# Kernel tuning notes

Measured on AMD Instinct MI355X. Metric: run time of the kernel, lower is better.

The kernel has to match this reference:

```python
import jax, jax.numpy as jnp
import numpy as np


def setup_inputs() -> dict:
    key = jax.random.key(0)
    k1, k2 = jax.random.split(key)
    N, M, C = 8192, 16384, 128
    features = jax.random.normal(k1, (N, 1, 1, C), dtype=jnp.float32)
    patch_memory = jax.random.normal(k2, (1, M, 1, C), dtype=jnp.float32)
    return {"features": features, "patch_memory": patch_memory}


def reference(features, patch_memory):
    # Faithful to: torch.norm(features - patch_memory, dim=3); torch.min(dim=1)
    # features: [N, 1, 1, C], patch_memory: [1, M, 1, C] -> broadcast diff [N, M, 1, C]
    # Avoid materializing the [N, M, C] diff tensor: use the GEMM expansion
    # ||a-b||^2 = ||a||^2 + ||b||^2 - 2 a.b (same math, efficient form).
    f = features.reshape(features.shape[0], features.shape[-1])       # [N, C]
    m = patch_memory.reshape(patch_memory.shape[1], patch_memory.shape[-1])  # [M, C]
    f2 = jnp.sum(f * f, axis=-1)   # [N]
    m2 = jnp.sum(m * m, axis=-1)   # [M]
    cross = jnp.einsum('nc,mc->nm', f, m)  # [N, M]
    d2 = f2[:, None] + m2[None, :] - 2.0 * cross
    distances = jnp.sqrt(jnp.maximum(d2, 0.0))       # [N, M] == norm over dim 3
    min_distances = jnp.min(distances, axis=1)       # min over memory dim (dim=1)
    # original keeps the trailing singleton patch dim -> [N, 1]
    return min_distances[:, None]
```

## Files before the change

kernel.cpp:

```cpp
#include <hip/hip_runtime.h>
#include <hip/hip_bf16.h>
#include <stdint.h>

#define N_ROWS 8192
#define M_ROWS 16384
#define CDIM 128
#define NTILE 16
#define BTROWS 128

typedef unsigned short u16;
typedef __attribute__((ext_vector_type(2))) unsigned short u16x2;
typedef __attribute__((ext_vector_type(8))) short bf16x8;
typedef __attribute__((ext_vector_type(4))) float f32x4;

static __device__ __forceinline__ u16 f2bf(float x) {
  union { float f; uint32_t u; } v; v.f = x;
  uint32_t u = v.u;
  uint32_t r = u + 0x7FFFu + ((u >> 16) & 1u);
  return (u16)(r >> 16);
}
static __device__ __forceinline__ float bf2f(u16 b) {
  union { uint32_t u; float f; } v; v.u = ((uint32_t)b) << 16;
  return v.f;
}

#define GLOAD_LDS(gsrc, ldst)                                                  \
  __builtin_amdgcn_global_load_lds(                                            \
      (const __attribute__((address_space(1))) uint32_t*)(gsrc),               \
      (__attribute__((address_space(3))) uint32_t*)(ldst), 16, 0, 0)

__global__ __launch_bounds__(256) void prep_kernel(
    const float* __restrict__ f, const float* __restrict__ m,
    u16* __restrict__ fb, u16* __restrict__ mb,
    float* __restrict__ f2, float* __restrict__ mh, int* __restrict__ mind2)
{
  const int row = blockIdx.x * 4 + (threadIdx.x >> 6);
  const int lane = threadIdx.x & 63;
  const bool isF = row < N_ROWS;
  const float* src = isF ? (f + (size_t)row * CDIM)
                         : (m + (size_t)(row - N_ROWS) * CDIM);
  float2 v = *(const float2*)(src + lane * 2);
  u16 b0 = f2bf(v.x), b1 = f2bf(v.y);
  float x0 = bf2f(b0), x1 = bf2f(b1);
  float s = x0 * x0 + x1 * x1;
#pragma unroll
  for (int mask = 1; mask < 64; mask <<= 1)
    s += __shfl_xor(s, mask, 64);
  u16x2 bb = {b0, b1};
  if (isF) {
    *(u16x2*)(fb + (size_t)row * CDIM + lane * 2) = bb;
    if (lane == 0) { f2[row] = s; mind2[row] = 0x7F7FFFFF; }
  } else {
    const int r = row - N_ROWS;
    *(u16x2*)(mb + (size_t)r * CDIM + lane * 2) = bb;
    if (lane == 0) mh[r] = -0.5f * s;
  }
}

__global__ __launch_bounds__(512, 2) void gemm_min_kernel(
    const u16* __restrict__ fb, const u16* __restrict__ mb,
    const float* __restrict__ f2, const float* __restrict__ mh,
    int* __restrict__ mind2)
{
  __shared__ __align__(16) u16 bts[3 * BTROWS * CDIM];
  __shared__ __align__(16) float mhl[2048];
  const int tid = threadIdx.x;
  const int msplit = blockIdx.x;
  const int nbase = blockIdx.y * 256;

  const int lane = tid & 63;
  const int w = tid >> 6;
  const int wm = w >> 1;
  const int wn = w & 1;
  const int l15 = lane & 15, l4 = lane >> 4;
  const int sw = (l15 & 7) << 4;

  {
    const u16* srcA = fb + (size_t)nbase * CDIM;
#pragma unroll
    for (int c = 0; c < 8; ++c) {
      const int t16 = c * 512 + tid;
      const int so = (t16 ^ ((t16 >> 4) & 7)) * 8;
      GLOAD_LDS(srcA + so, bts + t16 * 8);
    }
    GLOAD_LDS(mh + msplit * 2048 + tid * 4, mhl + tid * 4);
  }
  asm volatile("s_waitcnt vmcnt(0)" ::: "memory");
  __builtin_amdgcn_s_barrier();

  bf16x8 af[4][4];
#pragma unroll
  for (int mi = 0; mi < 4; ++mi)
#pragma unroll
    for (int ks = 0; ks < 4; ++ks) {
      const int row = wm * 64 + mi * 16 + l15;
      const int cb = (ks * 64 + l4 * 16) ^ sw;
      af[mi][ks] = *(const bf16x8*)&bts[row * CDIM + (cb >> 1)];
    }
  __syncthreads();

  const u16* mbase_ptr = mb + (size_t)(msplit * 2048) * CDIM;
#pragma unroll
  for (int tt = 0; tt < 2; ++tt)
#pragma unroll
    for (int c = 0; c < 4; ++c) {
      const int t16 = c * 512 + tid;
      const int so = (t16 ^ ((t16 >> 4) & 7)) * 8;
      GLOAD_LDS(mbase_ptr + (size_t)tt * BTROWS * CDIM + so,
                bts + tt * BTROWS * CDIM + t16 * 8);
    }
  asm volatile("s_waitcnt vmcnt(4)" ::: "memory");
  __builtin_amdgcn_s_barrier();

  float tmax[4][4];
#pragma unroll
  for (int mi = 0; mi < 4; ++mi)
#pragma unroll
    for (int j = 0; j < 4; ++j) tmax[mi][j] = -3.0e38f;

  f32x4 acc[4][4];
  int cur = 0;

  for (int t = 0; t < NTILE; ++t) {
    const u16* bt = bts + cur * BTROWS * CDIM;
    int stg = cur + 2; if (stg >= 3) stg -= 3;
    u16* stgbuf = bts + stg * BTROWS * CDIM;
    const u16* srcT2 = mbase_ptr + (size_t)((t + 2) & (NTILE - 1)) * BTROWS * CDIM;

#pragma unroll
    for (int p = 0; p < 4; ++p) {
      if (t) {
#pragma unroll
        for (int mi = 0; mi < 4; ++mi)
#pragma unroll
          for (int j = 0; j < 4; ++j)
            tmax[mi][j] = fmaxf(tmax[mi][j], acc[mi][p][j]);
      }
      const float mhv = mhl[t * BTROWS + wn * 64 + p * 16 + l15];
#pragma unroll
      for (int mi = 0; mi < 4; ++mi)
        acc[mi][p] = (f32x4){mhv, mhv, mhv, mhv};

      bf16x8 bg[4];
      {
        const int row = wn * 64 + p * 16 + l15;
#pragma unroll
        for (int ks = 0; ks < 4; ++ks) {
          const int cb = (ks * 64 + l4 * 16) ^ sw;
          bg[ks] = *(const bf16x8*)&bt[row * CDIM + (cb >> 1)];
        }
      }
      {
        const int t16 = p * 512 + tid;
        const int so = (t16 ^ ((t16 >> 4) & 7)) * 8;
        GLOAD_LDS(srcT2 + so, stgbuf + t16 * 8);
      }
      if (p == 3)
        asm volatile("s_waitcnt vmcnt(4)" ::: "memory");
      __builtin_amdgcn_s_barrier();
      __builtin_amdgcn_sched_barrier(0);
      __builtin_amdgcn_s_setprio(1);
#pragma unroll
      for (int ks = 0; ks < 4; ++ks)
#pragma unroll
        for (int mi = 0; mi < 4; ++mi)
          acc[mi][p] = __builtin_amdgcn_mfma_f32_16x16x32_bf16(
              af[mi][ks], bg[ks], acc[mi][p], 0, 0, 0);
      __builtin_amdgcn_s_setprio(0);
      __builtin_amdgcn_sched_barrier(0);
    }
    cur += 1; if (cur >= 3) cur -= 3;
  }

#pragma unroll
  for (int p = 0; p < 4; ++p)
#pragma unroll
    for (int mi = 0; mi < 4; ++mi)
#pragma unroll
      for (int j = 0; j < 4; ++j)
        tmax[mi][j] = fmaxf(tmax[mi][j], acc[mi][p][j]);

#pragma unroll
  for (int mi = 0; mi < 4; ++mi)
#pragma unroll
    for (int j = 0; j < 4; ++j) {
      float tv = tmax[mi][j];
      tv = fmaxf(tv, __shfl_xor(tv, 1, 64));
      tv = fmaxf(tv, __shfl_xor(tv, 2, 64));
      tv = fmaxf(tv, __shfl_xor(tv, 4, 64));
      tv = fmaxf(tv, __shfl_xor(tv, 8, 64));
      tmax[mi][j] = tv;
    }
  if (l15 == 0) {
#pragma unroll
    for (int mi = 0; mi < 4; ++mi)
#pragma unroll
      for (int j = 0; j < 4; ++j) {
        const int row = nbase + wm * 64 + mi * 16 + l4 * 4 + j;
        const float d2 = fmaxf(fmaf(-2.0f, tmax[mi][j], f2[row]), 0.0f);
        atomicMin(&mind2[row], __float_as_int(d2));
      }
  }
}

__global__ __launch_bounds__(256) void finalize_kernel(
    const int* __restrict__ mind2, float* __restrict__ out)
{
  const int i = blockIdx.x * 256 + threadIdx.x;
  out[i] = sqrtf(fmaxf(__int_as_float(mind2[i]), 0.0f));
}

extern "C" void kernel_launch(void* const* d_in, const int* in_sizes, int n_in,
                              void* d_out, int out_size, void* d_ws, size_t ws_size,
                              hipStream_t stream) {
  const float* f = (const float*)d_in[0];
  const float* m = (const float*)d_in[1];

  char* ws = (char*)d_ws;
  u16*  fb    = (u16*)(ws);
  u16*  mb    = (u16*)(ws + (2u << 20));
  float* f2   = (float*)(ws + (2u << 20) + (4u << 20));
  float* mh   = (float*)(ws + (2u << 20) + (4u << 20) + (32u << 10));
  int*  mind2 = (int*)(ws + (2u << 20) + (4u << 20) + (96u << 10));

  hipLaunchKernelGGL(prep_kernel, dim3((N_ROWS + M_ROWS) / 4), dim3(256), 0, stream,
                     f, m, fb, mb, f2, mh, mind2);
  hipLaunchKernelGGL(gemm_min_kernel, dim3(8, N_ROWS / 256), dim3(512), 0, stream,
                     fb, mb, f2, mh, mind2);
  hipLaunchKernelGGL(finalize_kernel, dim3(N_ROWS / 256), dim3(256), 0, stream,
                     mind2, (float*)d_out);
}
```

Baseline: 46.20 us.

## Switch to 32x32x16 MFMA with 128-row N tiles and 16-way LDS swizzle

The GEMM-min kernel now uses 32x32x16 bf16 MFMA instructions instead of 16x16x32. Each block covers 128 feature rows rather than 256, arranged as a 2x4 wave grid, and the grid doubles in the N dimension. The LDS swizzle widens to 16 chunks to suit the new fragment reads, and the four per-phase sub-steps collapse into one barrier per tile. This aims to cut LDS B-fragment traffic and barrier count per MFMA, at the cost of more blocks each re-streaming the memory bank and more atomics.

After: 70.43 us. 1.52x slower.

```diff
diff --git a/kernel.cpp b/kernel.cpp
--- a/kernel.cpp
+++ b/kernel.cpp
@@ -5,13 +5,14 @@
 #define N_ROWS 8192
 #define M_ROWS 16384
 #define CDIM 128
-#define NTILE 16
-#define BTROWS 128
+#define NT 16
+#define BTR 128
+#define TILE_U16 (BTR * CDIM)
 
 typedef unsigned short u16;
 typedef __attribute__((ext_vector_type(2))) unsigned short u16x2;
 typedef __attribute__((ext_vector_type(8))) short bf16x8;
-typedef __attribute__((ext_vector_type(4))) float f32x4;
+typedef __attribute__((ext_vector_type(16))) float f32x16;
 
 static __device__ __forceinline__ u16 f2bf(float x) {
   union { float f; uint32_t u; } v; v.f = x;
@@ -62,40 +63,45 @@
     const float* __restrict__ f2, const float* __restrict__ mh,
     int* __restrict__ mind2)
 {
-  __shared__ __align__(16) u16 bts[3 * BTROWS * CDIM];
+  __shared__ __align__(16) u16 bts[3 * TILE_U16];
   __shared__ __align__(16) float mhl[2048];
   const int tid = threadIdx.x;
   const int msplit = blockIdx.x;
-  const int nbase = blockIdx.y * 256;
+  const int nbase = blockIdx.y * 128;
 
   const int lane = tid & 63;
   const int w = tid >> 6;
-  const int wm = w >> 1;
-  const int wn = w & 1;
-  const int l15 = lane & 15, l4 = lane >> 4;
-  const int sw = (l15 & 7) << 4;
+  const int wm = w >> 2;
+  const int wn = w & 3;
+  const int l31 = lane & 31;
+  const int l5 = lane >> 5;
+  const int chSw = lane & 15;
+
+  int srcOffs[4], dstOffs[4];
+#pragma unroll
+  for (int c = 0; c < 4; ++c) {
+    const int t16 = c * 512 + tid;
+    srcOffs[c] = (t16 ^ ((t16 >> 4) & 15)) * 8;
+    dstOffs[c] = t16 * 8;
+  }
 
   {
     const u16* srcA = fb + (size_t)nbase * CDIM;
 #pragma unroll
-    for (int c = 0; c < 8; ++c) {
-      const int t16 = c * 512 + tid;
-      const int so = (t16 ^ ((t16 >> 4) & 7)) * 8;
-      GLOAD_LDS(srcA + so, bts + t16 * 8);
-    }
+    for (int c = 0; c < 4; ++c)
+      GLOAD_LDS(srcA + srcOffs[c], bts + dstOffs[c]);
     GLOAD_LDS(mh + msplit * 2048 + tid * 4, mhl + tid * 4);
   }
   asm volatile("s_waitcnt vmcnt(0)" ::: "memory");
   __builtin_amdgcn_s_barrier();
 
-  bf16x8 af[4][4];
-#pragma unroll
-  for (int mi = 0; mi < 4; ++mi)
-#pragma unroll
-    for (int ks = 0; ks < 4; ++ks) {
-      const int row = wm * 64 + mi * 16 + l15;
-      const int cb = (ks * 64 + l4 * 16) ^ sw;
-      af[mi][ks] = *(const bf16x8*)&bts[row * CDIM + (cb >> 1)];
+  bf16x8 af[2][8];
+#pragma unroll
+  for (int mi = 0; mi < 2; ++mi)
+#pragma unroll
+    for (int ks = 0; ks < 8; ++ks) {
+      const int row = wm * 64 + mi * 32 + l31;
+      af[mi][ks] = *(const bf16x8*)&bts[row * CDIM + (((ks * 2 + l5) ^ chSw) * 8)];
     }
   __syncthreads();
 
@@ -103,101 +109,92 @@
 #pragma unroll
   for (int tt = 0; tt < 2; ++tt)
 #pragma unroll
-    for (int c = 0; c < 4; ++c) {
-      const int t16 = c * 512 + tid;
-      const int so = (t16 ^ ((t16 >> 4) & 7)) * 8;
-      GLOAD_LDS(mbase_ptr + (size_t)tt * BTROWS * CDIM + so,
-                bts + tt * BTROWS * CDIM + t16 * 8);
-    }
+    for (int c = 0; c < 4; ++c)
+      GLOAD_LDS(mbase_ptr + (size_t)tt * TILE_U16 + srcOffs[c],
+                bts + tt * TILE_U16 + dstOffs[c]);
   asm volatile("s_waitcnt vmcnt(4)" ::: "memory");
   __builtin_amdgcn_s_barrier();
 
-  float tmax[4][4];
-#pragma unroll
-  for (int mi = 0; mi < 4; ++mi)
-#pragma unroll
-    for (int j = 0; j < 4; ++j) tmax[mi][j] = -3.0e38f;
-
-  f32x4 acc[4][4];
+  float tmax[2][16];
+#pragma unroll
+  for (int mi = 0; mi < 2; ++mi)
+#pragma unroll
+    for (int r = 0; r < 16; ++r) tmax[mi][r] = -3.0e38f;
+
+  f32x16 acc[2];
+  const int browL = wn * 32 + l31;
   int cur = 0;
 
-  for (int t = 0; t < NTILE; ++t) {
-    const u16* bt = bts + cur * BTROWS * CDIM;
+  for (int t = 0; t < NT; ++t) {
+    const u16* bt = bts + cur * TILE_U16;
     int stg = cur + 2; if (stg >= 3) stg -= 3;
-    u16* stgbuf = bts + stg * BTROWS * CDIM;
-    const u16* srcT2 = mbase_ptr + (size_t)((t + 2) & (NTILE - 1)) * BTROWS * CDIM;
-
-#pragma unroll
-    for (int p = 0; p < 4; ++p) {
-      if (t) {
-#pragma unroll
-        for (int mi = 0; mi < 4; ++mi)
-#pragma unroll
-          for (int j = 0; j < 4; ++j)
-            tmax[mi][j] = fmaxf(tmax[mi][j], acc[mi][p][j]);
-      }
-      const float mhv = mhl[t * BTROWS + wn * 64 + p * 16 + l15];
-#pragma unroll
-      for (int mi = 0; mi < 4; ++mi)
-        acc[mi][p] = (f32x4){mhv, mhv, mhv, mhv};
-
-      bf16x8 bg[4];
-      {
-        const int row = wn * 64 + p * 16 + l15;
-#pragma unroll
-        for (int ks = 0; ks < 4; ++ks) {
-          const int cb = (ks * 64 + l4 * 16) ^ sw;
-          bg[ks] = *(const bf16x8*)&bt[row * CDIM + (cb >> 1)];
-        }
-      }
-      {
-        const int t16 = p * 512 + tid;
-        const int so = (t16 ^ ((t16 >> 4) & 7)) * 8;
-        GLOAD_LDS(srcT2 + so, stgbuf + t16 * 8);
-      }
-      if (p == 3)
-        asm volatile("s_waitcnt vmcnt(4)" ::: "memory");
-      __builtin_amdgcn_s_barrier();
-      __builtin_amdgcn_sched_barrier(0);
-      __builtin_amdgcn_s_setprio(1);
-#pragma unroll
-      for (int ks = 0; ks < 4; ++ks)
-#pragma unroll
-        for (int mi = 0; mi < 4; ++mi)
-          acc[mi][p] = __builtin_amdgcn_mfma_f32_16x16x32_bf16(
-              af[mi][ks], bg[ks], acc[mi][p], 0, 0, 0);
-      __builtin_amdgcn_s_setprio(0);
-      __builtin_amdgcn_sched_barrier(0);
-    }
+    u16* stgbuf = bts + stg * TILE_U16;
+    const u16* srcT2 = mbase_ptr + (size_t)((t + 2) & (NT - 1)) * TILE_U16;
+
+    if (t) {
+#pragma unroll
+      for (int mi = 0; mi < 2; ++mi)
+#pragma unroll
+        for (int r = 0; r < 16; ++r)
+          tmax[mi][r] = fmaxf(tmax[mi][r], acc[mi][r]);
+    }
+    const float mhv = mhl[t * BTR + browL];
+#pragma unroll
+    for (int mi = 0; mi < 2; ++mi)
+#pragma unroll
+      for (int r = 0; r < 16; ++r) acc[mi][r] = mhv;
+
+    bf16x8 bg[8];
+    {
+      const u16* btrow = bt + browL * CDIM;
+#pragma unroll
+      for (int ks = 0; ks < 8; ++ks)
+        bg[ks] = *(const bf16x8*)&btrow[((ks * 2 + l5) ^ chSw) * 8];
+    }
+#pragma unroll
+    for (int c = 0; c < 4; ++c)
+      GLOAD_LDS(srcT2 + srcOffs[c], stgbuf + dstOffs[c]);
+
+    asm volatile("s_waitcnt vmcnt(4)" ::: "memory");
+    __builtin_amdgcn_s_barrier();
+
+    __builtin_amdgcn_s_setprio(1);
+#pragma unroll
+    for (int ks = 0; ks < 8; ++ks)
+#pragma unroll
+      for (int mi = 0; mi < 2; ++mi)
+        acc[mi] = __builtin_amdgcn_mfma_f32_32x32x16_bf16(
+            af[mi][ks], bg[ks], acc[mi], 0, 0, 0);
+    __builtin_amdgcn_s_setprio(0);
+
     cur += 1; if (cur >= 3) cur -= 3;
   }
 
 #pragma unroll
-  for (int p = 0; p < 4; ++p)
-#pragma unroll
-    for (int mi = 0; mi < 4; ++mi)
-#pragma unroll
-      for (int j = 0; j < 4; ++j)
-        tmax[mi][j] = fmaxf(tmax[mi][j], acc[mi][p][j]);
-
-#pragma unroll
-  for (int mi = 0; mi < 4; ++mi)
-#pragma unroll
-    for (int j = 0; j < 4; ++j) {
-      float tv = tmax[mi][j];
+  for (int mi = 0; mi < 2; ++mi)
+#pragma unroll
+    for (int r = 0; r < 16; ++r)
+      tmax[mi][r] = fmaxf(tmax[mi][r], acc[mi][r]);
+
+#pragma unroll
+  for (int mi = 0; mi < 2; ++mi)
+#pragma unroll
+    for (int r = 0; r < 16; ++r) {
+      float tv = tmax[mi][r];
       tv = fmaxf(tv, __shfl_xor(tv, 1, 64));
       tv = fmaxf(tv, __shfl_xor(tv, 2, 64));
       tv = fmaxf(tv, __shfl_xor(tv, 4, 64));
       tv = fmaxf(tv, __shfl_xor(tv, 8, 64));
-      tmax[mi][j] = tv;
-    }
-  if (l15 == 0) {
-#pragma unroll
-    for (int mi = 0; mi < 4; ++mi)
-#pragma unroll
-      for (int j = 0; j < 4; ++j) {
-        const int row = nbase + wm * 64 + mi * 16 + l4 * 4 + j;
-        const float d2 = fmaxf(fmaf(-2.0f, tmax[mi][j], f2[row]), 0.0f);
+      tv = fmaxf(tv, __shfl_xor(tv, 16, 64));
+      tmax[mi][r] = tv;
+    }
+  if (l31 == 0) {
+#pragma unroll
+    for (int mi = 0; mi < 2; ++mi)
+#pragma unroll
+      for (int r = 0; r < 16; ++r) {
+        const int row = nbase + wm * 64 + mi * 32 + (r & 3) + 8 * (r >> 2) + 4 * l5;
+        const float d2 = fmaxf(fmaf(-2.0f, tmax[mi][r], f2[row]), 0.0f);
         atomicMin(&mind2[row], __float_as_int(d2));
       }
   }
@@ -225,7 +222,7 @@
 
   hipLaunchKernelGGL(prep_kernel, dim3((N_ROWS + M_ROWS) / 4), dim3(256), 0, stream,
                      f, m, fb, mb, f2, mh, mind2);
-  hipLaunchKernelGGL(gemm_min_kernel, dim3(8, N_ROWS / 256), dim3(512), 0, stream,
+  hipLaunchKernelGGL(gemm_min_kernel, dim3(8, N_ROWS / 128), dim3(512), 0, stream,
                      fb, mb, f2, mh, mind2);
   hipLaunchKernelGGL(finalize_kernel, dim3(N_ROWS / 256), dim3(256), 0, stream,
                      mind2, (float*)d_out);
```
